# Performance work log

Hardware: AMD Instinct MI355X
Metric: run time of the kernel (lower is better)

## Reference

```python
import jax, jax.numpy as jnp
import numpy as np

L1, L2, ALPHA, BETA, EPS = 0.5, 1.5, 1.0, 50000000.0, 1e-08


def tube(att, label):
    # per-row cosine/sine TUBE distance, fully vectorized over batch
    dot = jnp.sum(att * label, axis=-1)            # [B]
    p_norm = jnp.sqrt(jnp.sum(att * att, axis=-1))
    g_norm = jnp.sqrt(jnp.sum(label * label, axis=-1))
    denom = p_norm * g_norm
    cosine = jnp.where(denom == 0, 0.0, dot / jnp.where(denom == 0, 1.0, denom))
    s_s = 1.0 - jnp.square(cosine)
    # s_s < 0 -> sine = 0 ; s_s == 0 -> sqrt(s_s + eps) ; else sqrt(s_s)
    sine = jnp.where(s_s < 0, 0.0, jnp.sqrt(jnp.where(s_s <= 0, EPS, s_s)))
    r_all = p_norm * cosine / jnp.where(g_norm == 0, g_norm + EPS, g_norm)
    base = p_norm * sine + jnp.abs(g_norm - p_norm * cosine)
    ds = jnp.where(r_all >= 1, L1 * base,
         jnp.where(r_all >= 0, base,
                   L2 * jnp.abs(p_norm * cosine - g_norm - p_norm * sine)))
    ds = -jnp.log(jnp.tanh(1.0 / ds))
    return jnp.mean(ds)


def kl_loss(mu, logvar):
    return -0.5 * BETA * jnp.mean(1.0 + logvar - jnp.square(mu) - jnp.exp(logvar))


def cross_entropy(logits, label_idx):
    logp = jax.nn.log_softmax(logits, axis=-1)
    return -jnp.mean(jnp.take_along_axis(logp, label_idx[:, None], axis=1)[:, 0])


def setup_inputs() -> dict:
    key = jax.random.key(0)
    ks = jax.random.split(key, 12)
    B, C, D, Z = 16384, 100, 512, 128
    return {
        "fusion_out": jax.random.normal(ks[0], (B, C), jnp.float32),
        "comple_out": jax.random.normal(ks[1], (B, D), jnp.float32),
        "labels": jax.random.normal(ks[2], (B, C), jnp.float32),
        "labels_encoder": jax.random.normal(ks[3], (B, D), jnp.float32),
        "x_A": jax.random.normal(ks[4], (B, D), jnp.float32),
        "x_A_reconstructed": jax.random.normal(ks[5], (B, D), jnp.float32),
        "x_B": jax.random.normal(ks[6], (B, D), jnp.float32),
        "x_B_reconstructed": jax.random.normal(ks[7], (B, D), jnp.float32),
        "x_C": jax.random.normal(ks[8], (B, D), jnp.float32),
        "x_C_reconstructed": jax.random.normal(ks[9], (B, D), jnp.float32),
        "mu": jax.random.normal(ks[10], (B, Z), jnp.float32),
        "logvar": jax.random.normal(ks[11], (B, Z), jnp.float32),
    }


def reference(fusion_out, comple_out, labels, labels_encoder, x_A,
              x_A_reconstructed, x_B, x_B_reconstructed, x_C,
              x_C_reconstructed, mu, logvar):
    label_idx = jnp.argmax(labels, axis=1)
    tube_A = ALPHA * tube(x_A_reconstructed, x_A)
    tube_B = ALPHA * tube(x_B_reconstructed, x_B)
    tube_C = ALPHA * tube(x_C_reconstructed, x_C)
    kl = kl_loss(mu, logvar)
    st_all = ALPHA * tube(comple_out, labels_encoder)
    ce = cross_entropy(fusion_out, label_idx)
    return tube_A + tube_B + tube_C + kl + ce + st_all
```

## Files before the change

### kernel.cpp

```cpp
#include <hip/hip_runtime.h>
#include <math.h>

static constexpr float kL1   = 0.5f;
static constexpr float kL2   = 1.5f;
static constexpr float kBeta = 50000000.0f;
static constexpr float kEps  = 1e-08f;

__device__ __forceinline__ float waveSum(float v) {
#pragma unroll
    for (int off = 32; off > 0; off >>= 1) v += __shfl_xor(v, off, 64);
    return v;
}

__global__ __launch_bounds__(256) void fused_loss_kernel(
    const float* __restrict__ fusion_out, const float* __restrict__ comple_out,
    const float* __restrict__ labels,     const float* __restrict__ labels_enc,
    const float* __restrict__ xA,  const float* __restrict__ xAr,
    const float* __restrict__ xB,  const float* __restrict__ xBr,
    const float* __restrict__ xC,  const float* __restrict__ xCr,
    const float* __restrict__ mu,  const float* __restrict__ logvar,
    float* __restrict__ out,
    int B, int C, int D, int Z,
    int tubeBlocks, int klBlocks, int ceBlocks)
{
    const int lane = threadIdx.x & 63;
    const int wave = threadIdx.x >> 6;
    const int wavesPerBlock = blockDim.x >> 6;
    const int bid = blockIdx.x;

    float my = 0.0f;

    if (bid < tubeBlocks) {
        const int globalWave = bid * wavesPerBlock + wave;
        const int totalWaves = tubeBlocks * wavesPerBlock;
        const int totalRows  = 4 * B;
        const int d4 = D >> 2;
        float acc = 0.0f;
        for (int row = globalWave; row < totalRows; row += totalWaves) {
            const int pair = row / B;
            const int r    = row - pair * B;
            const float* att; const float* lab;
            if      (pair == 0) { att = xAr;        lab = xA;         }
            else if (pair == 1) { att = xBr;        lab = xB;         }
            else if (pair == 2) { att = xCr;        lab = xC;         }
            else                { att = comple_out; lab = labels_enc; }
            const float4* a4 = (const float4*)(att + (size_t)r * D);
            const float4* l4 = (const float4*)(lab + (size_t)r * D);
            float dot = 0.f, pp = 0.f, gg = 0.f;
            for (int c = lane; c < d4; c += 64) {
                float4 a = a4[c];
                float4 l = l4[c];
                dot += a.x * l.x + a.y * l.y + a.z * l.z + a.w * l.w;
                pp  += a.x * a.x + a.y * a.y + a.z * a.z + a.w * a.w;
                gg  += l.x * l.x + l.y * l.y + l.z * l.z + l.w * l.w;
            }
            dot = waveSum(dot);
            pp  = waveSum(pp);
            gg  = waveSum(gg);
            if (lane == 0) {
                float p_norm = sqrtf(pp);
                float g_norm = sqrtf(gg);
                float denom  = p_norm * g_norm;
                float cosine = (denom == 0.0f) ? 0.0f : dot / denom;
                float s_s    = 1.0f - cosine * cosine;
                float sine   = (s_s < 0.0f) ? 0.0f
                             : sqrtf((s_s <= 0.0f) ? kEps : s_s);
                float gd     = (g_norm == 0.0f) ? (g_norm + kEps) : g_norm;
                float pc     = p_norm * cosine;
                float r_all  = pc / gd;
                float base   = p_norm * sine + fabsf(g_norm - pc);
                float ds     = (r_all >= 1.0f) ? (kL1 * base)
                             : ((r_all >= 0.0f) ? base
                                                : kL2 * fabsf(pc - g_norm - p_norm * sine));
                acc += -logf(tanhf(1.0f / ds));
            }
        }
        my = acc / (float)B;
    } else if (bid < tubeBlocks + klBlocks) {
        const int b2 = bid - tubeBlocks;
        const int n4 = (B * Z) >> 2;
        const float4* mu4 = (const float4*)mu;
        const float4* lv4 = (const float4*)logvar;
        const int tid    = b2 * blockDim.x + threadIdx.x;
        const int stride = klBlocks * blockDim.x;
        float acc = 0.0f;
        for (int i = tid; i < n4; i += stride) {
            float4 m = mu4[i];
            float4 l = lv4[i];
            acc += (1.0f + l.x - m.x * m.x - __expf(l.x));
            acc += (1.0f + l.y - m.y * m.y - __expf(l.y));
            acc += (1.0f + l.z - m.z * m.z - __expf(l.z));
            acc += (1.0f + l.w - m.w * m.w - __expf(l.w));
        }
        my = acc * (-0.5f * kBeta / (float)(B * Z));
    } else {
        const int b3 = bid - tubeBlocks - klBlocks;
        const int globalWave = b3 * wavesPerBlock + wave;
        const int totalWaves = ceBlocks * wavesPerBlock;
        float acc = 0.0f;
        for (int r = globalWave; r < B; r += totalWaves) {
            const float* lrow = labels     + (size_t)r * C;
            const float* frow = fusion_out + (size_t)r * C;
            const bool has0 = (lane < C);
            const bool has1 = (lane + 64 < C);
            float v0 = has0 ? lrow[lane]      : -INFINITY;
            float v1 = has1 ? lrow[lane + 64] : -INFINITY;
            float f0 = has0 ? frow[lane]      : -INFINITY;
            float f1 = has1 ? frow[lane + 64] : -INFINITY;
            float bv; int bi;
            if (v1 > v0) { bv = v1; bi = lane + 64; } else { bv = v0; bi = lane; }
#pragma unroll
            for (int off = 32; off > 0; off >>= 1) {
                float ov = __shfl_xor(bv, off, 64);
                int   oi = __shfl_xor(bi, off, 64);
                if (ov > bv || (ov == bv && oi < bi)) { bv = ov; bi = oi; }
            }
            float m = fmaxf(f0, f1);
#pragma unroll
            for (int off = 32; off > 0; off >>= 1) m = fmaxf(m, __shfl_xor(m, off, 64));
            float e = 0.0f;
            if (has0) e += __expf(f0 - m);
            if (has1) e += __expf(f1 - m);
            e = waveSum(e);
            float t = (bi < 64) ? __shfl(f0, bi, 64) : __shfl(f1, bi - 64, 64);
            if (lane == 0) acc += -(t - m - __logf(e));
        }
        my = acc / (float)B;
    }

    float s = waveSum(my);
    __shared__ float sw[8];
    if (lane == 0) sw[wave] = s;
    __syncthreads();
    if (threadIdx.x == 0) {
        float tot = 0.0f;
        for (int i = 0; i < wavesPerBlock; ++i) tot += sw[i];
        atomicAdd(out, tot);
    }
}

extern "C" void kernel_launch(void* const* d_in, const int* in_sizes, int n_in,
                              void* d_out, int out_size, void* d_ws, size_t ws_size,
                              hipStream_t stream) {
    const float* fusion_out = (const float*)d_in[0];
    const float* comple_out = (const float*)d_in[1];
    const float* labels     = (const float*)d_in[2];
    const float* labels_enc = (const float*)d_in[3];
    const float* xA  = (const float*)d_in[4];
    const float* xAr = (const float*)d_in[5];
    const float* xB  = (const float*)d_in[6];
    const float* xBr = (const float*)d_in[7];
    const float* xC  = (const float*)d_in[8];
    const float* xCr = (const float*)d_in[9];
    const float* mu  = (const float*)d_in[10];
    const float* lv  = (const float*)d_in[11];
    float* out = (float*)d_out;

    const int B = 16384;
    const int C = in_sizes[0] / B;
    const int D = in_sizes[1] / B;
    const int Z = in_sizes[10] / B;

    const int tubeBlocks = 4096;
    const int klBlocks   = 512;
    const int ceBlocks   = 512;
    const int totalBlocks = tubeBlocks + klBlocks + ceBlocks;

    hipMemsetAsync(out, 0, sizeof(float), stream);
    fused_loss_kernel<<<totalBlocks, 256, 0, stream>>>(
        fusion_out, comple_out, labels, labels_enc,
        xA, xAr, xB, xBr, xC, xCr, mu, lv,
        out, B, C, D, Z, tubeBlocks, klBlocks, ceBlocks);
}
```

Before: 299.9 us.

## Process two tube rows per wave, use fast log-tanh, and reduce partials deterministically

Each tube wave now processes two rows per iteration with D hardcoded to 512, issuing all eight float4 loads up front and interleaving the six shuffle reductions to increase memory-level parallelism. The -log(tanh(x)) tail is rewritten with fast exp/log intrinsics. CE blocks increase from 512 to 2048. The global atomicAdd and memset are replaced by per-block partials written to workspace and summed by a second single-block kernel. These trade generality (fixed D and B as power of two) and an extra launch for fewer serialized atomics and more loads in flight.

Result: faster. 288.1 us (-4.0%).

```diff
diff --git a/kernel.cpp b/kernel.cpp
--- a/kernel.cpp
+++ b/kernel.cpp
@@ -12,21 +12,41 @@
     return v;
 }
 
-__global__ __launch_bounds__(256) void fused_loss_kernel(
+__device__ __forceinline__ float tubeTail(float dot, float pp, float gg) {
+    float p_norm = sqrtf(pp);
+    float g_norm = sqrtf(gg);
+    float denom  = p_norm * g_norm;
+    float cosine = (denom == 0.0f) ? 0.0f : dot / denom;
+    float s_s    = 1.0f - cosine * cosine;
+    float sine   = (s_s < 0.0f) ? 0.0f : sqrtf((s_s <= 0.0f) ? kEps : s_s);
+    float gd     = (g_norm == 0.0f) ? (g_norm + kEps) : g_norm;
+    float pc     = p_norm * cosine;
+    float r_all  = pc / gd;
+    float base   = p_norm * sine + fabsf(g_norm - pc);
+    float ds     = (r_all >= 1.0f) ? (kL1 * base)
+                 : ((r_all >= 0.0f) ? base
+                                    : kL2 * fabsf(pc - g_norm - p_norm * sine));
+    float t  = 1.0f / ds;
+    float em = __expf(-2.0f * t);
+    return __logf(1.0f + em) - __logf(fmaxf(1.0f - em, 1e-30f));
+}
+
+__global__ __launch_bounds__(256) void fused_loss_partials(
     const float* __restrict__ fusion_out, const float* __restrict__ comple_out,
     const float* __restrict__ labels,     const float* __restrict__ labels_enc,
     const float* __restrict__ xA,  const float* __restrict__ xAr,
     const float* __restrict__ xB,  const float* __restrict__ xBr,
     const float* __restrict__ xC,  const float* __restrict__ xCr,
     const float* __restrict__ mu,  const float* __restrict__ logvar,
-    float* __restrict__ out,
-    int B, int C, int D, int Z,
+    float* __restrict__ partials,
+    int B, int C, int Z,
     int tubeBlocks, int klBlocks, int ceBlocks)
 {
     const int lane = threadIdx.x & 63;
     const int wave = threadIdx.x >> 6;
     const int wavesPerBlock = blockDim.x >> 6;
     const int bid = blockIdx.x;
+    const int D = 512;
 
     float my = 0.0f;
 
@@ -34,45 +54,45 @@
         const int globalWave = bid * wavesPerBlock + wave;
         const int totalWaves = tubeBlocks * wavesPerBlock;
         const int totalRows  = 4 * B;
-        const int d4 = D >> 2;
+        const float* atts[4] = { xAr, xBr, xCr, comple_out };
+        const float* labs[4] = { xA,  xB,  xC,  labels_enc  };
         float acc = 0.0f;
-        for (int row = globalWave; row < totalRows; row += totalWaves) {
-            const int pair = row / B;
-            const int r    = row - pair * B;
-            const float* att; const float* lab;
-            if      (pair == 0) { att = xAr;        lab = xA;         }
-            else if (pair == 1) { att = xBr;        lab = xB;         }
-            else if (pair == 2) { att = xCr;        lab = xC;         }
-            else                { att = comple_out; lab = labels_enc; }
-            const float4* a4 = (const float4*)(att + (size_t)r * D);
-            const float4* l4 = (const float4*)(lab + (size_t)r * D);
-            float dot = 0.f, pp = 0.f, gg = 0.f;
-            for (int c = lane; c < d4; c += 64) {
-                float4 a = a4[c];
-                float4 l = l4[c];
-                dot += a.x * l.x + a.y * l.y + a.z * l.z + a.w * l.w;
-                pp  += a.x * a.x + a.y * a.y + a.z * a.z + a.w * a.w;
-                gg  += l.x * l.x + l.y * l.y + l.z * l.z + l.w * l.w;
+        for (int row = globalWave; row < totalRows; row += 2 * totalWaves) {
+            const int row2 = row + totalWaves;
+            const int p0 = row  >> 14, r0 = row  & (B - 1);
+            const int p1 = row2 >> 14, r1 = row2 & (B - 1);
+            const float4* a0 = (const float4*)(atts[p0] + (size_t)r0 * D);
+            const float4* l0 = (const float4*)(labs[p0] + (size_t)r0 * D);
+            const float4* a1 = (const float4*)(atts[p1] + (size_t)r1 * D);
+            const float4* l1 = (const float4*)(labs[p1] + (size_t)r1 * D);
+            float4 A0 = a0[lane], A1 = a0[lane + 64];
+            float4 L0 = l0[lane], L1 = l0[lane + 64];
+            float4 A2 = a1[lane], A3 = a1[lane + 64];
+            float4 L2 = l1[lane], L3 = l1[lane + 64];
+            float dotA = A0.x*L0.x + A0.y*L0.y + A0.z*L0.z + A0.w*L0.w
+                       + A1.x*L1.x + A1.y*L1.y + A1.z*L1.z + A1.w*L1.w;
+            float ppA  = A0.x*A0.x + A0.y*A0.y + A0.z*A0.z + A0.w*A0.w
+                       + A1.x*A1.x + A1.y*A1.y + A1.z*A1.z + A1.w*A1.w;
+            float ggA  = L0.x*L0.x + L0.y*L0.y + L0.z*L0.z + L0.w*L0.w
+                       + L1.x*L1.x + L1.y*L1.y + L1.z*L1.z + L1.w*L1.w;
+            float dotB = A2.x*L2.x + A2.y*L2.y + A2.z*L2.z + A2.w*L2.w
+                       + A3.x*L3.x + A3.y*L3.y + A3.z*L3.z + A3.w*L3.w;
+            float ppB  = A2.x*A2.x + A2.y*A2.y + A2.z*A2.z + A2.w*A2.w
+                       + A3.x*A3.x + A3.y*A3.y + A3.z*A3.z + A3.w*A3.w;
+            float ggB  = L2.x*L2.x + L2.y*L2.y + L2.z*L2.z + L2.w*L2.w
+                       + L3.x*L3.x + L3.y*L3.y + L3.z*L3.z + L3.w*L3.w;
+#pragma unroll
+            for (int off = 32; off > 0; off >>= 1) {
+                dotA += __shfl_xor(dotA, off, 64);
+                ppA  += __shfl_xor(ppA,  off, 64);
+                ggA  += __shfl_xor(ggA,  off, 64);
+                dotB += __shfl_xor(dotB, off, 64);
+                ppB  += __shfl_xor(ppB,  off, 64);
+                ggB  += __shfl_xor(ggB,  off, 64);
             }
-            dot = waveSum(dot);
-            pp  = waveSum(pp);
-            gg  = waveSum(gg);
             if (lane == 0) {
-                float p_norm = sqrtf(pp);
-                float g_norm = sqrtf(gg);
-                float denom  = p_norm * g_norm;
-                float cosine = (denom == 0.0f) ? 0.0f : dot / denom;
-                float s_s    = 1.0f - cosine * cosine;
-                float sine   = (s_s < 0.0f) ? 0.0f
-                             : sqrtf((s_s <= 0.0f) ? kEps : s_s);
-                float gd     = (g_norm == 0.0f) ? (g_norm + kEps) : g_norm;
-                float pc     = p_norm * cosine;
-                float r_all  = pc / gd;
-                float base   = p_norm * sine + fabsf(g_norm - pc);
-                float ds     = (r_all >= 1.0f) ? (kL1 * base)
-                             : ((r_all >= 0.0f) ? base
-                                                : kL2 * fabsf(pc - g_norm - p_norm * sine));
-                acc += -logf(tanhf(1.0f / ds));
+                acc += tubeTail(dotA, ppA, ggA);
+                acc += tubeTail(dotB, ppB, ggB);
             }
         }
         my = acc / (float)B;
@@ -135,8 +155,22 @@
     if (threadIdx.x == 0) {
         float tot = 0.0f;
         for (int i = 0; i < wavesPerBlock; ++i) tot += sw[i];
-        atomicAdd(out, tot);
+        partials[bid] = tot;
     }
+}
+
+__global__ __launch_bounds__(256) void reduce_partials(
+    const float* __restrict__ partials, float* __restrict__ out, int n)
+{
+    float s = 0.0f;
+    for (int i = threadIdx.x; i < n; i += 256) s += partials[i];
+    s = waveSum(s);
+    __shared__ float sw[4];
+    const int lane = threadIdx.x & 63;
+    const int wave = threadIdx.x >> 6;
+    if (lane == 0) sw[wave] = s;
+    __syncthreads();
+    if (threadIdx.x == 0) out[0] = sw[0] + sw[1] + sw[2] + sw[3];
 }
 
 extern "C" void kernel_launch(void* const* d_in, const int* in_sizes, int n_in,
@@ -155,20 +189,20 @@
     const float* mu  = (const float*)d_in[10];
     const float* lv  = (const float*)d_in[11];
     float* out = (float*)d_out;
+    float* ws  = (float*)d_ws;
 
     const int B = 16384;
     const int C = in_sizes[0] / B;
-    const int D = in_sizes[1] / B;
     const int Z = in_sizes[10] / B;
 
     const int tubeBlocks = 4096;
     const int klBlocks   = 512;
-    const int ceBlocks   = 512;
+    const int ceBlocks   = 2048;
     const int totalBlocks = tubeBlocks + klBlocks + ceBlocks;
 
-    hipMemsetAsync(out, 0, sizeof(float), stream);
-    fused_loss_kernel<<<totalBlocks, 256, 0, stream>>>(
+    fused_loss_partials<<<totalBlocks, 256, 0, stream>>>(
         fusion_out, comple_out, labels, labels_enc,
         xA, xAr, xB, xBr, xC, xCr, mu, lv,
-        out, B, C, D, Z, tubeBlocks, klBlocks, ceBlocks);
-}
+        ws, B, C, Z, tubeBlocks, klBlocks, ceBlocks);
+    reduce_partials<<<1, 256, 0, stream>>>(ws, out, totalBlocks);
+}
```
